# Optimization experiments

Hardware: AMD Instinct MI355X
Metric: run time of the kernel (lower is better)

Reference implementation:

```python
import jax, jax.numpy as jnp
import numpy as np

# Static config (matches init_kwargs)
B = 1
D = 1024          # model_dim
H = 16            # num_heads
HD = 64           # head_dim
TPF = 256         # tokens_per_frame = latent_height*latent_width
LH, LW = 16, 16
FRAMES = 13
PREFIX = 1
ATTN = 3
CHUNKS = 4
TXT = 226                 # text_length per chunk
SEQ_TXT = CHUNKS * TXT    # 904
VID_LEN = FRAMES * TPF    # 3328
CHUNK_VID = (PREFIX + ATTN) * TPF  # 1024 video tokens per attention chunk
THETA = 10000.0
EPS = 1e-6
SCALE = 1.0 / np.sqrt(HD)
DT, DHE, DW = 16, 24, 24  # 3D rope split of head_dim


def setup_inputs() -> dict:
    key = jax.random.key(0)
    ks = jax.random.split(key, 16)
    def w(k, shape, s=0.02):
        return (jax.random.normal(k, shape) * s).astype(jnp.float32)
    return dict(
        vid_emb=jax.random.normal(ks[0], (B, VID_LEN, D), jnp.float32),
        text_emb=jax.random.normal(ks[1], (B, SEQ_TXT, D), jnp.float32),
        Wq=w(ks[2], (D, D)), bq=jnp.zeros((D,), jnp.float32),
        Wk=w(ks[3], (D, D)), bk=jnp.zeros((D,), jnp.float32),
        Wv=w(ks[4], (D, D)), bv=jnp.zeros((D,), jnp.float32),
        Wo=w(ks[5], (D, D)), bo=jnp.zeros((D,), jnp.float32),
        qn_w=jnp.ones((HD,), jnp.float32), qn_b=jnp.zeros((HD,), jnp.float32),
        kn_w=jnp.ones((HD,), jnp.float32), kn_b=jnp.zeros((HD,), jnp.float32),
        ssm_Win=w(ks[6], (D, D)), ssm_Wout=w(ks[7], (D, D)),
        ssm_gate=jnp.zeros((D,), jnp.float32),
        fg_t=jnp.full((D,), 0.1, jnp.float32), fg_v=jnp.full((D,), 0.1, jnp.float32),
        bg_t=jnp.full((D,), 0.1, jnp.float32), bg_v=jnp.full((D,), 0.1, jnp.float32),
    )


def _layernorm(x, w, b):
    mu = jnp.mean(x, axis=-1, keepdims=True)
    var = jnp.mean((x - mu) ** 2, axis=-1, keepdims=True)
    return (x - mu) * jax.lax.rsqrt(var + EPS) * w + b


def _rope_angles():
    # per-video-token 3D positions within a chunk
    tok = jnp.arange(CHUNK_VID)
    f = (tok // TPF).astype(jnp.float32)
    rem = tok % TPF
    hp = (rem // LW).astype(jnp.float32)
    wp = (rem % LW).astype(jnp.float32)
    def inv(d):
        return THETA ** (-jnp.arange(0, d, 2, dtype=jnp.float32) / d)
    return f[:, None] * inv(DT), hp[:, None] * inv(DHE), wp[:, None] * inv(DW)


def _rot(x, ang):
    half = x.shape[-1] // 2
    c, s = jnp.cos(ang), jnp.sin(ang)
    x1, x2 = x[..., :half], x[..., half:]
    return jnp.concatenate([x1 * c - x2 * s, x1 * s + x2 * c], axis=-1)


def _apply_rope3d(x, angs):
    at, ah, aw = angs
    return jnp.concatenate([
        _rot(x[..., :DT], at),
        _rot(x[..., DT:DT + DHE], ah),
        _rot(x[..., DT + DHE:], aw),
    ], axis=-1)


def _attn_forward(vid_emb, text_emb, Wq, bq, Wk, bk, Wv, bv, Wo, bo, qn_w, qn_b, kn_w, kn_b):
    b = vid_emb.shape[0]
    starts = np.arange(CHUNKS) * ATTN * TPF
    idx = jnp.asarray(starts)[:, None] + jnp.arange(CHUNK_VID)[None, :]  # [C, CHUNK_VID]
    txt_chunks = text_emb.reshape(b, CHUNKS, TXT, D)
    vid_chunks = vid_emb[:, idx]                                          # [b, C, CHUNK_VID, D]
    cur = jnp.concatenate([txt_chunks, vid_chunks], axis=2)               # [b, C, T, D]
    T = TXT + CHUNK_VID
    cur = cur.reshape(b * CHUNKS, T, D)

    def heads(x):
        return x.reshape(b * CHUNKS, T, H, HD).transpose(0, 2, 1, 3)      # [bc, h, t, d]

    q = _layernorm(heads(cur @ Wq + bq), qn_w, qn_b)
    k = _layernorm(heads(cur @ Wk + bk), kn_w, kn_b)
    v = heads(cur @ Wv + bv)

    angs = _rope_angles()
    q = jnp.concatenate([q[:, :, :TXT], _apply_rope3d(q[:, :, TXT:], angs)], axis=2)
    k = jnp.concatenate([k[:, :, :TXT], _apply_rope3d(k[:, :, TXT:], angs)], axis=2)

    scores = jnp.einsum('bhqd,bhkd->bhqk', q, k) * SCALE
    attn = jax.nn.softmax(scores, axis=-1)
    out = jnp.einsum('bhqk,bhkd->bhqd', attn, v)
    out = out.transpose(0, 2, 1, 3).reshape(b * CHUNKS, T, D) @ Wo + bo
    out = out.reshape(b, CHUNKS, T, D)

    text_out = out[:, :, :TXT].reshape(b, SEQ_TXT, D)
    vid_part = out[:, :, TXT:]                                            # [b, C, CHUNK_VID, D]
    vid_acc = jnp.zeros((b, VID_LEN, D), vid_emb.dtype).at[:, idx].add(vid_part)
    cnt = jnp.zeros((b, VID_LEN, 1), vid_emb.dtype).at[:, idx].add(jnp.ones((b, CHUNKS, CHUNK_VID, 1), vid_emb.dtype))
    vid_out = vid_acc / cnt
    return jnp.concatenate([text_out, vid_out], axis=1)


def _ssm(x, Win, Wout, gate_logit):
    # simplified TTT stand-in: gated linear recurrence h_t = g*h_{t-1} + u_t (causal scan)
    g = jax.nn.sigmoid(gate_logit)
    u = x @ Win
    a = jnp.broadcast_to(g, u.shape)
    def comb(c1, c2):
        a1, b1 = c1
        a2, b2 = c2
        return a1 * a2, a2 * b1 + b2
    _, h = jax.lax.associative_scan(comb, (a, u), axis=1)
    return h @ Wout


def _rev_text_chunks(t):
    b = t.shape[0]
    return jnp.flip(t.reshape(b, CHUNKS, TXT, D), axis=1).reshape(b, SEQ_TXT, D)


def _ssm_forward(emb, ssm_Win, ssm_Wout, ssm_gate, fg_t, fg_v, bg_t, bg_v):
    Ttxt = SEQ_TXT
    res = emb
    y = _ssm(emb, ssm_Win, ssm_Wout, ssm_gate)
    emb = res + jnp.concatenate([jnp.tanh(fg_t) * y[:, :Ttxt], jnp.tanh(fg_v) * y[:, Ttxt:]], axis=1)
    res2 = emb
    # multiscene reverse: flip text chunk order and video token order
    rev = jnp.concatenate([_rev_text_chunks(emb[:, :Ttxt]), jnp.flip(emb[:, Ttxt:], axis=1)], axis=1)
    y2 = _ssm(rev, ssm_Win, ssm_Wout, ssm_gate)
    y2 = jnp.concatenate([_rev_text_chunks(y2[:, :Ttxt]), jnp.flip(y2[:, Ttxt:], axis=1)], axis=1)
    return res2 + jnp.concatenate([jnp.tanh(bg_t) * y2[:, :Ttxt], jnp.tanh(bg_v) * y2[:, Ttxt:]], axis=1)


def reference(vid_emb, text_emb, Wq, bq, Wk, bk, Wv, bv, Wo, bo, qn_w, qn_b, kn_w, kn_b,
              ssm_Win, ssm_Wout, ssm_gate, fg_t, fg_v, bg_t, bg_v):
    emb = _attn_forward(vid_emb, text_emb, Wq, bq, Wk, bk, Wv, bv, Wo, bo, qn_w, qn_b, kn_w, kn_b)
    out = _ssm_forward(emb, ssm_Win, ssm_Wout, ssm_gate, fg_t, fg_v, bg_t, bg_v)
    return out[:, SEQ_TXT:], out[:, :SEQ_TXT]
```

## Files before the change

kernel.cpp:

```cpp
#include <hip/hip_runtime.h>
#include <cstdint>

constexpr int Dm       = 1024;
constexpr int Hh       = 16;
constexpr int HD       = 64;
constexpr int CHUNKS   = 4;
constexpr int TXT      = 226;
constexpr int SEQ_TXT  = 904;
constexpr int VID_LEN  = 3328;
constexpr int CHUNK_VID= 1024;
constexpr int Tt       = 1250;
constexpr int Tp       = 1280;
constexpr int M_QKV    = 5000;
constexpr int SEQm     = 4232;
constexpr int STRIDE_V = 768;
constexpr float EPSc   = 1e-6f;
constexpr float SCALEc = 0.125f;
constexpr float THETAc = 10000.f;
constexpr float OFFS   = 8.0f;

constexpr int SEGL = 128;
constexpr int NSEG = (SEQm + SEGL - 1) / SEGL;

typedef __attribute__((ext_vector_type(8))) short bf16x8;
typedef __attribute__((ext_vector_type(4))) float f32x4;

__device__ __forceinline__ ushort f2bf(float x) {
    uint32_t u = __float_as_uint(x);
    u += 0x7FFFu + ((u >> 16) & 1u);
    return (ushort)(u >> 16);
}
__device__ __forceinline__ float bf2f(ushort b) {
    return __uint_as_float(((uint32_t)b) << 16);
}

__device__ __forceinline__ void gload_lds16(const ushort* g, ushort* l) {
    __builtin_amdgcn_global_load_lds(
        (const __attribute__((address_space(1))) unsigned int*)g,
        (__attribute__((address_space(3))) unsigned int*)l, 16, 0, 0);
}

__device__ __forceinline__ int rev_map(int i) {
    if (i < SEQ_TXT) {
        int c = i / TXT, o = i - c * TXT;
        return (CHUNKS - 1 - c) * TXT + o;
    }
    int j = i - SEQ_TXT;
    return SEQ_TXT + (VID_LEN - 1 - j);
}

__global__ __launch_bounds__(256) void conv_w_all(
    const float* __restrict__ Wq, const float* __restrict__ Wk,
    const float* __restrict__ Wv, const float* __restrict__ Wo,
    const float* __restrict__ Win, const float* __restrict__ Wout,
    ushort* __restrict__ WqkvH, ushort* __restrict__ WqkvL,
    ushort* __restrict__ WoH, ushort* __restrict__ WoL,
    ushort* __restrict__ WinH, ushort* __restrict__ WinL,
    ushort* __restrict__ WoutH, ushort* __restrict__ WoutL) {
    const float* W; ushort* Thi; ushort* Tlo;
    switch (blockIdx.z) {
        case 0: W = Wq;  Thi = WqkvH;               Tlo = WqkvL;               break;
        case 1: W = Wk;  Thi = WqkvH + 1024*1024;   Tlo = WqkvL + 1024*1024;   break;
        case 2: W = Wv;  Thi = WqkvH + 2*1024*1024; Tlo = WqkvL + 2*1024*1024; break;
        case 3: W = Wo;  Thi = WoH;   Tlo = WoL;   break;
        case 4: W = Win; Thi = WinH;  Tlo = WinL;  break;
        default:W = Wout;Thi = WoutH; Tlo = WoutL; break;
    }
    __shared__ float tile[32][33];
    int k0 = blockIdx.y * 32, n0 = blockIdx.x * 32;
    int j = threadIdx.x & 31, i0 = threadIdx.x >> 5;
#pragma unroll
    for (int i = i0; i < 32; i += 8)
        tile[i][j] = W[(size_t)(k0 + i) * 1024 + n0 + j];
    __syncthreads();
#pragma unroll
    for (int i = i0; i < 32; i += 8) {
        float v = tile[j][i];
        ushort h = f2bf(v);
        size_t o = (size_t)(n0 + i) * 1024 + k0 + j;
        Thi[o] = h;
        Tlo[o] = f2bf(v - bf2f(h));
    }
}

__global__ __launch_bounds__(256) void build_cur(
    const float* __restrict__ vid, const float* __restrict__ txt,
    ushort* __restrict__ chi, ushort* __restrict__ clo) {
    int idx = blockIdx.x * 256 + threadIdx.x;
    int row = idx >> 8, c4 = (idx & 255) * 4;
    int c = row / Tt, t = row - c * Tt;
    float4 x;
    if (t < TXT)
        x = *(const float4*)(txt + (size_t)(c * TXT + t) * Dm + c4);
    else
        x = *(const float4*)(vid + (size_t)(c * STRIDE_V + (t - TXT)) * Dm + c4);
    float v[4] = {x.x, x.y, x.z, x.w};
    ushort4 h, l;
    h.x = f2bf(v[0]); l.x = f2bf(v[0] - bf2f(h.x));
    h.y = f2bf(v[1]); l.y = f2bf(v[1] - bf2f(h.y));
    h.z = f2bf(v[2]); l.z = f2bf(v[2] - bf2f(h.z));
    h.w = f2bf(v[3]); l.w = f2bf(v[3] - bf2f(h.w));
    *(ushort4*)(chi + (size_t)row * Dm + c4) = h;
    *(ushort4*)(clo + (size_t)row * Dm + c4) = l;
}

template<int MODE>
__global__ __launch_bounds__(256) void gemm_sk(
    const ushort* __restrict__ Ahi, const ushort* __restrict__ Alo,
    const ushort* __restrict__ Bhi, const ushort* __restrict__ Blo,
    const float* __restrict__ f1, const float* __restrict__ f2,
    const float* __restrict__ f3,
    const ushort* __restrict__ r1, const ushort* __restrict__ r2,
    float* __restrict__ Cf, ushort* __restrict__ u1, ushort* __restrict__ u2,
    int M, int N) {
    __shared__ ushort AHL[128 * 64];
    __shared__ ushort BHL[128 * 64];
    const int tid = threadIdx.x;
    const int w = tid >> 6, lane = tid & 63;
    const int lrow = lane & 15, quad = lane >> 4;
    const int mBase = blockIdx.y * 128, nBase = blockIdx.x * 128;

    const bool isB = (w >= 2);
    const int half = w & 1;
    const ushort* Phi = isB ? Bhi : Ahi;
    const ushort* Plo = isB ? Blo : Alo;
    ushort* lds = (isB ? BHL : AHL) + half * 4096;
    const int baseR = (isB ? nBase : mBase) + half * 64;
    const int maxr = (isB ? N : M) - 1;
    const int rl8 = lane >> 3;
    const int c = (lane & 7) ^ rl8;
    const ushort* Psel = (c < 4) ? Phi : Plo;
    const ushort* gb[8];
#pragma unroll
    for (int u = 0; u < 8; ++u) {
        int rg = min(baseR + u * 8 + rl8, maxr);
        gb[u] = Psel + (size_t)rg * 1024 + (c & 3) * 8;
    }

    const int mo = (w >> 1) * 64, no = (w & 1) * 64;
    const int p = quad ^ (lrow & 7);
    f32x4 acc[4][4];
#pragma unroll
    for (int i = 0; i < 4; ++i)
#pragma unroll
        for (int j = 0; j < 4; ++j) acc[i][j] = (f32x4){0.f, 0.f, 0.f, 0.f};

    for (int kk = 0; kk < 1024; kk += 32) {
        __syncthreads();
#pragma unroll
        for (int u = 0; u < 8; ++u) gload_lds16(gb[u] + kk, lds + u * 512);
        __syncthreads();

        bf16x8 ah[4], al[4], bh[4], bl[4];
#pragma unroll
        for (int i = 0; i < 4; ++i) {
            int m = mo + i * 16 + lrow;
            ah[i] = *(const bf16x8*)&AHL[m * 64 + p * 8];
            al[i] = *(const bf16x8*)&AHL[m * 64 + (p ^ 4) * 8];
        }
#pragma unroll
        for (int j = 0; j < 4; ++j) {
            int n = no + j * 16 + lrow;
            bh[j] = *(const bf16x8*)&BHL[n * 64 + p * 8];
            bl[j] = *(const bf16x8*)&BHL[n * 64 + (p ^ 4) * 8];
        }
#pragma unroll
        for (int i = 0; i < 4; ++i)
#pragma unroll
            for (int j = 0; j < 4; ++j) {
                f32x4 a = acc[i][j];
                a = __builtin_amdgcn_mfma_f32_16x16x32_bf16(ah[i], bh[j], a, 0, 0, 0);
                a = __builtin_amdgcn_mfma_f32_16x16x32_bf16(al[i], bh[j], a, 0, 0, 0);
                a = __builtin_amdgcn_mfma_f32_16x16x32_bf16(ah[i], bl[j], a, 0, 0, 0);
                acc[i][j] = a;
            }
    }

#pragma unroll
    for (int i = 0; i < 4; ++i)
#pragma unroll
        for (int j = 0; j < 4; ++j) {
            const int col = nBase + no + j * 16 + lrow;
            float bv = 0.f, tg_t = 0.f, tg_v = 0.f;
            if constexpr (MODE == 0) bv = f1[col];
            if constexpr (MODE == 1)
                bv = (col < 1024) ? f1[col]
                   : (col < 2048) ? f2[col - 1024] : f3[col - 2048];
            if constexpr (MODE == 3 || MODE == 4) {
                tg_t = tanhf(f1[col]);
                tg_v = tanhf(f2[col]);
            }
#pragma unroll
            for (int r = 0; r < 4; ++r) {
                const int row = mBase + mo + i * 16 + quad * 4 + r;
                if (row >= M) continue;
                const size_t idx = (size_t)row * N + col;
                const float a = acc[i][j][r];
                if constexpr (MODE == 0) {
                    Cf[idx] = a + bv;
                } else if constexpr (MODE == 1) {
                    u1[idx] = f2bf(a + bv);
                } else if constexpr (MODE == 2) {
                    Cf[idx] = a;
                } else if constexpr (MODE == 3) {
                    float e = bf2f(r1[idx]) + bf2f(r2[idx]);
                    float g = (row < SEQ_TXT) ? tg_t : tg_v;
                    float v = e + g * a;
                    Cf[idx] = v;
                    ushort hh = f2bf(v);
                    u1[idx] = hh;
                    u2[idx] = f2bf(v - bf2f(hh));
                } else {
                    float e = f3[idx];
                    float g = (row < SEQ_TXT) ? tg_t : tg_v;
                    int drow = (row >= SEQ_TXT) ? (row - SEQ_TXT) : (VID_LEN + row);
                    Cf[(size_t)drow * N + col] = e + g * a;
                }
            }
        }
}

__global__ __launch_bounds__(256) void lnrope(
    const ushort* __restrict__ qkvb,
    const float* __restrict__ qn_w, const float* __restrict__ qn_b,
    const float* __restrict__ kn_w, const float* __restrict__ kn_b,
    ushort* __restrict__ qP, ushort* __restrict__ kP, ushort* __restrict__ vT) {
    __shared__ ushort vtile[64][72];
    const int ch = blockIdx.y, c = ch >> 4, h = ch & 15;
    const int t0 = blockIdx.x * 64;
    const int tid = threadIdx.x, w = tid >> 6, lane = tid & 63;

    auto wsum = [](float x) {
#pragma unroll
        for (int o = 32; o; o >>= 1) x += __shfl_xor(x, o);
        return x;
    };

#pragma unroll 1
    for (int it = 0; it < 16; ++it) {
        const int tl = w * 16 + it;
        const int t = t0 + tl;
        ushort qb = 0, kb = 0, vb = 0;
        if (t < Tt) {
            size_t src = (size_t)(c * Tt + t) * 3072 + h * HD + lane;
            float qv = bf2f(qkvb[src]);
            float kv = bf2f(qkvb[src + 1024]);
            float vv = bf2f(qkvb[src + 2048]);

            float qmu = wsum(qv) * (1.f / 64.f);
            float qd  = qv - qmu;
            float qvar = wsum(qd * qd) * (1.f / 64.f);
            float qn = qd * rsqrtf(qvar + EPSc) * qn_w[lane] + qn_b[lane];

            float kmu = wsum(kv) * (1.f / 64.f);
            float kd  = kv - kmu;
            float kvar = wsum(kd * kd) * (1.f / 64.f);
            float kn = kd * rsqrtf(kvar + EPSc) * kn_w[lane] + kn_b[lane];

            if (t >= TXT) {
                int pos = t - TXT;
                int f = pos >> 8, rem2 = pos & 255, hp = rem2 >> 4, wp = rem2 & 15;
                int dim, pp, dl;
                if (lane < 16)      { dim = 16; pp = f;  dl = lane; }
                else if (lane < 40) { dim = 24; pp = hp; dl = lane - 16; }
                else                { dim = 24; pp = wp; dl = lane - 40; }
                int halfd = dim >> 1;
                int i = (dl < halfd) ? dl : dl - halfd;
                float ang = (float)pp * powf(THETAc, -2.0f * (float)i / (float)dim);
                float cs = cosf(ang), sn = sinf(ang);
                int partner = (dl < halfd) ? (lane + halfd) : (lane - halfd);
                float qo = __shfl(qn, partner);
                float ko = __shfl(kn, partner);
                qn = (dl < halfd) ? (qn * cs - qo * sn) : (qo * sn + qn * cs);
                kn = (dl < halfd) ? (kn * cs - ko * sn) : (ko * sn + kn * cs);
            }
            qb = f2bf(qn * SCALEc);
            kb = f2bf(kn);
            vb = f2bf(vv);
        }
        size_t dst = ((size_t)ch * Tp + t) * HD + lane;
        qP[dst] = qb;
        kP[dst] = kb;
        vtile[tl][lane] = vb;
    }
    __syncthreads();
    const int r = tid >> 2, ck = tid & 3;
    ushort* dst = vT + ((size_t)ch * HD + r) * Tp + t0;
    short o1[8], o2[8];
#pragma unroll
    for (int j = 0; j < 8; ++j) {
        o1[j] = (short)vtile[ck * 8 + j][r];
        o2[j] = (short)vtile[(ck + 4) * 8 + j][r];
    }
    *(bf16x8*)(dst + ck * 8)       = *(bf16x8*)o1;
    *(bf16x8*)(dst + (ck + 4) * 8) = *(bf16x8*)o2;
}

__global__ __launch_bounds__(256) void attn_mfma(
    const ushort* __restrict__ qP, const ushort* __restrict__ kP,
    const ushort* __restrict__ vT,
    ushort* __restrict__ ohi, ushort* __restrict__ olo) {
    const int ch = blockIdx.y;
    const int c = ch >> 4, h = ch & 15;
    const int qbase = blockIdx.x * 64;
    const int tid = threadIdx.x, w = tid >> 6, lane = tid & 63;
    const int lrow = lane & 15, quad = lane >> 4;

    __shared__ ushort KT[2][32 * 64];
    __shared__ ushort VTs[2][64 * 32];
    __shared__ ushort PB[4][16][40];

    const ushort* kg = kP + (size_t)ch * Tp * HD;
    const ushort* vg = vT + (size_t)ch * HD * Tp;

    const ushort* kgl = kg + (size_t)(w * 8 + (lane >> 3)) * HD
                           + ((lane & 7) ^ ((lane >> 3) & 7)) * 8;
    const ushort* vgl = vg + (size_t)(w * 16 + (lane >> 2)) * Tp + (lane & 3) * 8;

    const int qr = qbase + w * 16 + lrow;
    const ushort* qgp = qP + ((size_t)ch * Tp + qr) * HD + quad * 8;
    bf16x8 qf0 = *(const bf16x8*)qgp;
    bf16x8 qf1 = *(const bf16x8*)(qgp + 32);

    f32x4 accO[4];
#pragma unroll
    for (int dt = 0; dt < 4; ++dt) accO[dt] = (f32x4){0.f, 0.f, 0.f, 0.f};
    float lacc[4] = {0.f, 0.f, 0.f, 0.f};

    gload_lds16(kgl, &KT[0][w * 512]);
    gload_lds16(vgl, &VTs[0][w * 512]);

    const int NSTEP = Tp / 32;
    for (int s = 0; s < NSTEP; ++s) {
        const int b = s & 1;
        __syncthreads();
        if (s + 1 < NSTEP) {
            int kb = (s + 1) * 32;
            gload_lds16(kgl + (size_t)kb * HD, &KT[1 - b][w * 512]);
            gload_lds16(vgl + kb, &VTs[1 - b][w * 512]);
        }

        const int sw = lrow & 7;
        const ushort* r0 = &KT[b][lrow * 64];
        const ushort* r1 = &KT[b][(16 + lrow) * 64];
        bf16x8 k00 = *(const bf16x8*)(r0 + (quad ^ sw) * 8);
        bf16x8 k01 = *(const bf16x8*)(r0 + ((4 + quad) ^ sw) * 8);
        bf16x8 k10 = *(const bf16x8*)(r1 + (quad ^ sw) * 8);
        bf16x8 k11 = *(const bf16x8*)(r1 + ((4 + quad) ^ sw) * 8);
        f32x4 s0 = (f32x4){0.f, 0.f, 0.f, 0.f}, s1 = s0;
        s0 = __builtin_amdgcn_mfma_f32_16x16x32_bf16(qf0, k00, s0, 0, 0, 0);
        s0 = __builtin_amdgcn_mfma_f32_16x16x32_bf16(qf1, k01, s0, 0, 0, 0);
        s1 = __builtin_amdgcn_mfma_f32_16x16x32_bf16(qf0, k10, s1, 0, 0, 0);
        s1 = __builtin_amdgcn_mfma_f32_16x16x32_bf16(qf1, k11, s1, 0, 0, 0);

#pragma unroll
        for (int r = 0; r < 4; ++r) {
            float p0 = __expf(s0[r] - OFFS);
            float p1 = __expf(s1[r] - OFFS);
            lacc[r] += p0 + p1;
            int row = quad * 4 + r;
            PB[w][row][lrow]      = f2bf(p0);
            PB[w][row][16 + lrow] = f2bf(p1);
        }

        bf16x8 pf = *(const bf16x8*)&PB[w][lrow][quad * 8];
#pragma unroll
        for (int dt = 0; dt < 4; ++dt) {
            bf16x8 vf = *(const bf16x8*)&VTs[b][(dt * 16 + lrow) * 32 + quad * 8];
            accO[dt] = __builtin_amdgcn_mfma_f32_16x16x32_bf16(pf, vf, accO[dt], 0, 0, 0);
        }
    }

    float il[4];
#pragma unroll
    for (int r = 0; r < 4; ++r) {
        float l = lacc[r];
        l += __shfl_xor(l, 1);
        l += __shfl_xor(l, 2);
        l += __shfl_xor(l, 4);
        l += __shfl_xor(l, 8);
        l -= (float)(Tp - Tt) * __expf(-OFFS);
        il[r] = 1.f / l;
    }
#pragma unroll
    for (int dt = 0; dt < 4; ++dt)
#pragma unroll
        for (int r = 0; r < 4; ++r) {
            int qrow = qbase + w * 16 + quad * 4 + r;
            if (qrow < Tt) {
                float val = accO[dt][r] * il[r];
                size_t o = (size_t)(c * Tt + qrow) * Dm + h * HD + dt * 16 + lrow;
                ushort hv = f2bf(val);
                ohi[o] = hv;
                olo[o] = f2bf(val - bf2f(hv));
            }
        }
}

__global__ __launch_bounds__(256) void scatter_emb(
    const float* __restrict__ proj,
    ushort* __restrict__ ehi, ushort* __restrict__ elo) {
    int idx = blockIdx.x * 256 + threadIdx.x;
    int row = idx >> 8, c4 = (idx & 255) * 4;
    float4 o;
    if (row < SEQ_TXT) {
        int c = row / TXT, t = row - c * TXT;
        o = *(const float4*)(proj + (size_t)(c * Tt + t) * Dm + c4);
    } else {
        int p = row - SEQ_TXT;
        float sx = 0.f, sy = 0.f, sz = 0.f, sw = 0.f; int cnt = 0;
#pragma unroll
        for (int c = 0; c < CHUNKS; ++c) {
            int off = p - c * STRIDE_V;
            if (off >= 0 && off < CHUNK_VID) {
                float4 x = *(const float4*)(proj + (size_t)(c * Tt + TXT + off) * Dm + c4);
                sx += x.x; sy += x.y; sz += x.z; sw += x.w; ++cnt;
            }
        }
        float inv = 1.f / (float)cnt;
        o = make_float4(sx * inv, sy * inv, sz * inv, sw * inv);
    }
    float v[4] = {o.x, o.y, o.z, o.w};
    ushort4 h, l;
    h.x = f2bf(v[0]); l.x = f2bf(v[0] - bf2f(h.x));
    h.y = f2bf(v[1]); l.y = f2bf(v[1] - bf2f(h.y));
    h.z = f2bf(v[2]); l.z = f2bf(v[2] - bf2f(h.z));
    h.w = f2bf(v[3]); l.w = f2bf(v[3] - bf2f(h.w));
    *(ushort4*)(ehi + (size_t)row * Dm + c4) = h;
    *(ushort4*)(elo + (size_t)row * Dm + c4) = l;
}

__global__ __launch_bounds__(256) void scan_carry(
    const float* __restrict__ u, const float* __restrict__ gate,
    float* __restrict__ carry, int perm) {
    int ch = blockIdx.x * 256 + threadIdx.x;
    int seg = blockIdx.y;
    float g = 1.f / (1.f + expf(-gate[ch]));
    int t0 = seg * SEGL, t1 = min(SEQm, t0 + SEGL);
    float hv = 0.f;
    for (int t = t0; t < t1; ++t) {
        int rt = perm ? rev_map(t) : t;
        hv = fmaf(g, hv, u[(size_t)rt * Dm + ch]);
    }
    carry[(size_t)seg * Dm + ch] = hv;
}

__global__ __launch_bounds__(256) void scan_combine(
    const float* __restrict__ carry, const float* __restrict__ gate,
    float* __restrict__ inc) {
    int ch = blockIdx.x * 256 + threadIdx.x;
    float g = 1.f / (1.f + expf(-gate[ch]));
    float gl = powf(g, (float)SEGL);
    float S = 0.f;
    for (int s = 0; s < NSEG; ++s) {
        inc[(size_t)s * Dm + ch] = S;
        int len = min(SEGL, SEQm - s * SEGL);
        float A = (len == SEGL) ? gl : powf(g, (float)len);
        S = fmaf(A, S, carry[(size_t)s * Dm + ch]);
    }
}

__global__ __launch_bounds__(256) void scan_final(
    const float* __restrict__ u, const float* __restrict__ gate,
    const float* __restrict__ inc,
    ushort* __restrict__ hhi, ushort* __restrict__ hlo, int perm) {
    int ch = blockIdx.x * 256 + threadIdx.x;
    int seg = blockIdx.y;
    float g = 1.f / (1.f + expf(-gate[ch]));
    int t0 = seg * SEGL, t1 = min(SEQm, t0 + SEGL);
    float hv = inc[(size_t)seg * Dm + ch];
    for (int t = t0; t < t1; ++t) {
        int rt = perm ? rev_map(t) : t;
        hv = fmaf(g, hv, u[(size_t)rt * Dm + ch]);
        ushort h = f2bf(hv);
        hhi[(size_t)rt * Dm + ch] = h;
        hlo[(size_t)rt * Dm + ch] = f2bf(hv - bf2f(h));
    }
}

extern "C" void kernel_launch(void* const* d_in, const int* in_sizes, int n_in,
                              void* d_out, int out_size, void* d_ws, size_t ws_size,
                              hipStream_t stream) {
    const float* vid_emb = (const float*)d_in[0];
    const float* text_emb= (const float*)d_in[1];
    const float* Wq = (const float*)d_in[2];  const float* bq = (const float*)d_in[3];
    const float* Wk = (const float*)d_in[4];  const float* bk = (const float*)d_in[5];
    const float* Wv = (const float*)d_in[6];  const float* bv = (const float*)d_in[7];
    const float* Wo = (const float*)d_in[8];  const float* bo = (const float*)d_in[9];
    const float* qn_w = (const float*)d_in[10]; const float* qn_b = (const float*)d_in[11];
    const float* kn_w = (const float*)d_in[12]; const float* kn_b = (const float*)d_in[13];
    const float* Win  = (const float*)d_in[14]; const float* Wout = (const float*)d_in[15];
    const float* gate = (const float*)d_in[16];
    const float* fg_t = (const float*)d_in[17]; const float* fg_v = (const float*)d_in[18];
    const float* bg_t = (const float*)d_in[19]; const float* bg_v = (const float*)d_in[20];

    char* W8 = (char*)d_ws;
    if (ws_size < 132284416u) return;
    ushort* WqkvH = (ushort*)(W8 + 0);
    ushort* WqkvL = (ushort*)(W8 + 6291456);
    ushort* WoH   = (ushort*)(W8 + 12582912);
    ushort* WoL   = (ushort*)(W8 + 14680064);
    ushort* WinH  = (ushort*)(W8 + 16777216);
    ushort* WinL  = (ushort*)(W8 + 18874368);
    ushort* WoutH = (ushort*)(W8 + 20971520);
    ushort* WoutL = (ushort*)(W8 + 23068672);
    ushort* qkvb  = (ushort*)(W8 + 25165824);
    ushort* curH  = (ushort*)(W8 + 55885824);
    ushort* curL  = (ushort*)(W8 + 66125824);
    ushort* qPl   = (ushort*)(W8 + 76365824);
    ushort* kPl   = (ushort*)(W8 + 86851584);
    ushort* vTl   = (ushort*)(W8 + 97337344);
    ushort* aoutH = (ushort*)(W8 + 25165824);
    ushort* aoutL = (ushort*)(W8 + 35405824);
    float*  proj  = (float*) (W8 + 55885824);
    ushort* embH  = (ushort*)(W8 + 25165824);
    ushort* embL  = (ushort*)(W8 + 33832960);
    float*  u     = (float*) (W8 + 55885824);
    ushort* hbufH = (ushort*)(W8 + 76365824);
    ushort* hbufL = (ushort*)(W8 + 85032960);
    float*  emb2  = (float*) (W8 + 97337344);
    ushort* e2H   = (ushort*)(W8 + 114671616);
    ushort* e2L   = (ushort*)(W8 + 123338752);
    float*  carry = (float*) (W8 + 132005888);
    float*  incb  = (float*) (W8 + 132145152);
    float*  outp  = (float*)d_out;

    conv_w_all<<<dim3(32, 32, 6), 256, 0, stream>>>(
        Wq, Wk, Wv, Wo, Win, Wout,
        WqkvH, WqkvL, WoH, WoL, WinH, WinL, WoutH, WoutL);

    build_cur<<<M_QKV, 256, 0, stream>>>(vid_emb, text_emb, curH, curL);

    gemm_sk<1><<<dim3(24, 40), 256, 0, stream>>>(
        curH, curL, WqkvH, WqkvL, bq, bk, bv, nullptr, nullptr,
        nullptr, qkvb, nullptr, M_QKV, 3072);

    lnrope<<<dim3(Tp / 64, 64), 256, 0, stream>>>(qkvb, qn_w, qn_b, kn_w, kn_b,
                                                  qPl, kPl, vTl);

    attn_mfma<<<dim3(Tp / 64, 64), 256, 0, stream>>>(qPl, kPl, vTl, aoutH, aoutL);

    gemm_sk<0><<<dim3(8, 40), 256, 0, stream>>>(
        aoutH, aoutL, WoH, WoL, bo, nullptr, nullptr, nullptr, nullptr,
        proj, nullptr, nullptr, M_QKV, 1024);

    scatter_emb<<<SEQm, 256, 0, stream>>>(proj, embH, embL);

    dim3 gsq(8, 34);
    dim3 gscan(Dm / 256, NSEG);

    gemm_sk<2><<<gsq, 256, 0, stream>>>(
        embH, embL, WinH, WinL, nullptr, nullptr, nullptr, nullptr, nullptr,
        u, nullptr, nullptr, SEQm, 1024);
    scan_carry<<<gscan, 256, 0, stream>>>(u, gate, carry, 0);
    scan_combine<<<Dm / 256, 256, 0, stream>>>(carry, gate, incb);
    scan_final<<<gscan, 256, 0, stream>>>(u, gate, incb, hbufH, hbufL, 0);
    gemm_sk<3><<<gsq, 256, 0, stream>>>(
        hbufH, hbufL, WoutH, WoutL, fg_t, fg_v, nullptr, embH, embL,
        emb2, e2H, e2L, SEQm, 1024);

    gemm_sk<2><<<gsq, 256, 0, stream>>>(
        e2H, e2L, WinH, WinL, nullptr, nullptr, nullptr, nullptr, nullptr,
        u, nullptr, nullptr, SEQm, 1024);
    scan_carry<<<gscan, 256, 0, stream>>>(u, gate, carry, 1);
    scan_combine<<<Dm / 256, 256, 0, stream>>>(carry, gate, incb);
    scan_final<<<gscan, 256, 0, stream>>>(u, gate, incb, hbufH, hbufL, 1);
    gemm_sk<4><<<gsq, 256, 0, stream>>>(
        hbufH, hbufL, WoutH, WoutL, bg_t, bg_v, emb2, nullptr, nullptr,
        outp, nullptr, nullptr, SEQm, 1024);
}
```

Before: 774.6 us.

## Split-K the N=1024 GEMMs in two and fold reductions into epilogue kernels

The 1024-wide GEMMs (Wo, SSM Win and Wout) now run as split-K with two K halves on blockIdx.z, each writing its own fp32 partial buffer. This doubles the grid from about 272-320 to 544-640 blocks so the many CUs stay busy. The partial sums are added inside the consumers: scan_carry and scan_final, a new reduce_scatter that also adds the bias, and new reduce_c1 and reduce_fin kernels that apply the gated residual. The cost is an extra fp32 partial write and read, and two more launches. The workspace buffers are remapped to fit the larger partials.

```diff
diff --git a/kernel.cpp b/kernel.cpp
--- a/kernel.cpp
+++ b/kernel.cpp
@@ -110,8 +110,7 @@
     const ushort* __restrict__ Bhi, const ushort* __restrict__ Blo,
     const float* __restrict__ f1, const float* __restrict__ f2,
     const float* __restrict__ f3,
-    const ushort* __restrict__ r1, const ushort* __restrict__ r2,
-    float* __restrict__ Cf, ushort* __restrict__ u1, ushort* __restrict__ u2,
+    float* __restrict__ Cf, ushort* __restrict__ u1,
     int M, int N) {
     __shared__ ushort AHL[128 * 64];
     __shared__ ushort BHL[128 * 64];
@@ -145,7 +144,9 @@
 #pragma unroll
         for (int j = 0; j < 4; ++j) acc[i][j] = (f32x4){0.f, 0.f, 0.f, 0.f};
 
-    for (int kk = 0; kk < 1024; kk += 32) {
+    const int kk0 = (MODE == 5) ? blockIdx.z * 512 : 0;
+    const int kk1 = (MODE == 5) ? kk0 + 512 : 1024;
+    for (int kk = kk0; kk < kk1; kk += 32) {
         __syncthreads();
 #pragma unroll
         for (int u = 0; u < 8; ++u) gload_lds16(gb[u] + kk, lds + u * 512);
@@ -176,45 +177,26 @@
             }
     }
 
+    const size_t zoff = (MODE == 5) ? (size_t)blockIdx.z * M * N : 0;
 #pragma unroll
     for (int i = 0; i < 4; ++i)
 #pragma unroll
         for (int j = 0; j < 4; ++j) {
             const int col = nBase + no + j * 16 + lrow;
-            float bv = 0.f, tg_t = 0.f, tg_v = 0.f;
-            if constexpr (MODE == 0) bv = f1[col];
+            float bv = 0.f;
             if constexpr (MODE == 1)
                 bv = (col < 1024) ? f1[col]
                    : (col < 2048) ? f2[col - 1024] : f3[col - 2048];
-            if constexpr (MODE == 3 || MODE == 4) {
-                tg_t = tanhf(f1[col]);
-                tg_v = tanhf(f2[col]);
-            }
 #pragma unroll
             for (int r = 0; r < 4; ++r) {
                 const int row = mBase + mo + i * 16 + quad * 4 + r;
                 if (row >= M) continue;
                 const size_t idx = (size_t)row * N + col;
                 const float a = acc[i][j][r];
-                if constexpr (MODE == 0) {
-                    Cf[idx] = a + bv;
-                } else if constexpr (MODE == 1) {
+                if constexpr (MODE == 1) {
                     u1[idx] = f2bf(a + bv);
-                } else if constexpr (MODE == 2) {
-                    Cf[idx] = a;
-                } else if constexpr (MODE == 3) {
-                    float e = bf2f(r1[idx]) + bf2f(r2[idx]);
-                    float g = (row < SEQ_TXT) ? tg_t : tg_v;
-                    float v = e + g * a;
-                    Cf[idx] = v;
-                    ushort hh = f2bf(v);
-                    u1[idx] = hh;
-                    u2[idx] = f2bf(v - bf2f(hh));
                 } else {
-                    float e = f3[idx];
-                    float g = (row < SEQ_TXT) ? tg_t : tg_v;
-                    int drow = (row >= SEQ_TXT) ? (row - SEQ_TXT) : (VID_LEN + row);
-                    Cf[(size_t)drow * N + col] = e + g * a;
+                    Cf[zoff + idx] = a;
                 }
             }
         }
@@ -397,30 +379,39 @@
         }
 }
 
-__global__ __launch_bounds__(256) void scatter_emb(
-    const float* __restrict__ proj,
+__global__ __launch_bounds__(256) void reduce_scatter(
+    const float* __restrict__ P0, const float* __restrict__ bo,
     ushort* __restrict__ ehi, ushort* __restrict__ elo) {
+    const float* P1 = P0 + (size_t)M_QKV * Dm;
     int idx = blockIdx.x * 256 + threadIdx.x;
     int row = idx >> 8, c4 = (idx & 255) * 4;
-    float4 o;
+    float sx, sy, sz, sw;
     if (row < SEQ_TXT) {
         int c = row / TXT, t = row - c * TXT;
-        o = *(const float4*)(proj + (size_t)(c * Tt + t) * Dm + c4);
+        size_t o = (size_t)(c * Tt + t) * Dm + c4;
+        float4 a = *(const float4*)(P0 + o);
+        float4 b = *(const float4*)(P1 + o);
+        sx = a.x + b.x; sy = a.y + b.y; sz = a.z + b.z; sw = a.w + b.w;
     } else {
         int p = row - SEQ_TXT;
-        float sx = 0.f, sy = 0.f, sz = 0.f, sw = 0.f; int cnt = 0;
+        sx = sy = sz = sw = 0.f; int cnt = 0;
 #pragma unroll
         for (int c = 0; c < CHUNKS; ++c) {
             int off = p - c * STRIDE_V;
             if (off >= 0 && off < CHUNK_VID) {
-                float4 x = *(const float4*)(proj + (size_t)(c * Tt + TXT + off) * Dm + c4);
-                sx += x.x; sy += x.y; sz += x.z; sw += x.w; ++cnt;
+                size_t o = (size_t)(c * Tt + TXT + off) * Dm + c4;
+                float4 a = *(const float4*)(P0 + o);
+                float4 b = *(const float4*)(P1 + o);
+                sx += a.x + b.x; sy += a.y + b.y;
+                sz += a.z + b.z; sw += a.w + b.w;
+                ++cnt;
             }
         }
         float inv = 1.f / (float)cnt;
-        o = make_float4(sx * inv, sy * inv, sz * inv, sw * inv);
-    }
-    float v[4] = {o.x, o.y, o.z, o.w};
+        sx *= inv; sy *= inv; sz *= inv; sw *= inv;
+    }
+    float4 b4 = *(const float4*)(bo + c4);
+    float v[4] = {sx + b4.x, sy + b4.y, sz + b4.z, sw + b4.w};
     ushort4 h, l;
     h.x = f2bf(v[0]); l.x = f2bf(v[0] - bf2f(h.x));
     h.y = f2bf(v[1]); l.y = f2bf(v[1] - bf2f(h.y));
@@ -431,8 +422,9 @@
 }
 
 __global__ __launch_bounds__(256) void scan_carry(
-    const float* __restrict__ u, const float* __restrict__ gate,
+    const float* __restrict__ P0, const float* __restrict__ gate,
     float* __restrict__ carry, int perm) {
+    const float* P1 = P0 + (size_t)SEQm * Dm;
     int ch = blockIdx.x * 256 + threadIdx.x;
     int seg = blockIdx.y;
     float g = 1.f / (1.f + expf(-gate[ch]));
@@ -440,7 +432,8 @@
     float hv = 0.f;
     for (int t = t0; t < t1; ++t) {
         int rt = perm ? rev_map(t) : t;
-        hv = fmaf(g, hv, u[(size_t)rt * Dm + ch]);
+        size_t o = (size_t)rt * Dm + ch;
+        hv = fmaf(g, hv, P0[o] + P1[o]);
     }
     carry[(size_t)seg * Dm + ch] = hv;
 }
@@ -461,9 +454,10 @@
 }
 
 __global__ __launch_bounds__(256) void scan_final(
-    const float* __restrict__ u, const float* __restrict__ gate,
+    const float* __restrict__ P0, const float* __restrict__ gate,
     const float* __restrict__ inc,
     ushort* __restrict__ hhi, ushort* __restrict__ hlo, int perm) {
+    const float* P1 = P0 + (size_t)SEQm * Dm;
     int ch = blockIdx.x * 256 + threadIdx.x;
     int seg = blockIdx.y;
     float g = 1.f / (1.f + expf(-gate[ch]));
@@ -471,11 +465,61 @@
     float hv = inc[(size_t)seg * Dm + ch];
     for (int t = t0; t < t1; ++t) {
         int rt = perm ? rev_map(t) : t;
-        hv = fmaf(g, hv, u[(size_t)rt * Dm + ch]);
+        size_t o = (size_t)rt * Dm + ch;
+        hv = fmaf(g, hv, P0[o] + P1[o]);
         ushort h = f2bf(hv);
-        hhi[(size_t)rt * Dm + ch] = h;
-        hlo[(size_t)rt * Dm + ch] = f2bf(hv - bf2f(h));
-    }
+        hhi[o] = h;
+        hlo[o] = f2bf(hv - bf2f(h));
+    }
+}
+
+__global__ __launch_bounds__(256) void reduce_c1(
+    const float* __restrict__ P0,
+    const ushort* __restrict__ ehi, const ushort* __restrict__ elo,
+    const float* __restrict__ fg_t, const float* __restrict__ fg_v,
+    float* __restrict__ emb2, ushort* __restrict__ e2hi, ushort* __restrict__ e2lo) {
+    const float* P1 = P0 + (size_t)SEQm * Dm;
+    int idx = blockIdx.x * 256 + threadIdx.x;
+    int row = idx >> 8, c4 = (idx & 255) * 4;
+    const float* fg = (row < SEQ_TXT) ? fg_t : fg_v;
+    size_t o = (size_t)row * Dm + c4;
+    float4 a = *(const float4*)(P0 + o);
+    float4 b = *(const float4*)(P1 + o);
+    ushort4 eh = *(const ushort4*)(ehi + o);
+    ushort4 el = *(const ushort4*)(elo + o);
+    float v[4];
+    v[0] = (bf2f(eh.x) + bf2f(el.x)) + tanhf(fg[c4 + 0]) * (a.x + b.x);
+    v[1] = (bf2f(eh.y) + bf2f(el.y)) + tanhf(fg[c4 + 1]) * (a.y + b.y);
+    v[2] = (bf2f(eh.z) + bf2f(el.z)) + tanhf(fg[c4 + 2]) * (a.z + b.z);
+    v[3] = (bf2f(eh.w) + bf2f(el.w)) + tanhf(fg[c4 + 3]) * (a.w + b.w);
+    *(float4*)(emb2 + o) = make_float4(v[0], v[1], v[2], v[3]);
+    ushort4 h, l;
+    h.x = f2bf(v[0]); l.x = f2bf(v[0] - bf2f(h.x));
+    h.y = f2bf(v[1]); l.y = f2bf(v[1] - bf2f(h.y));
+    h.z = f2bf(v[2]); l.z = f2bf(v[2] - bf2f(h.z));
+    h.w = f2bf(v[3]); l.w = f2bf(v[3] - bf2f(h.w));
+    *(ushort4*)(e2hi + o) = h;
+    *(ushort4*)(e2lo + o) = l;
+}
+
+__global__ __launch_bounds__(256) void reduce_fin(
+    const float* __restrict__ P0, const float* __restrict__ emb2,
+    const float* __restrict__ bg_t, const float* __restrict__ bg_v,
+    float* __restrict__ outp) {
+    const float* P1 = P0 + (size_t)SEQm * Dm;
+    int idx = blockIdx.x * 256 + threadIdx.x;
+    int row = idx >> 8, c4 = (idx & 255) * 4;
+    const float* bg = (row < SEQ_TXT) ? bg_t : bg_v;
+    int drow = (row >= SEQ_TXT) ? (row - SEQ_TXT) : (VID_LEN + row);
+    size_t o = (size_t)row * Dm + c4;
+    float4 a = *(const float4*)(P0 + o);
+    float4 b = *(const float4*)(P1 + o);
+    float4 e = *(const float4*)(emb2 + o);
+    float4 r = make_float4(e.x + tanhf(bg[c4 + 0]) * (a.x + b.x),
+                           e.y + tanhf(bg[c4 + 1]) * (a.y + b.y),
+                           e.z + tanhf(bg[c4 + 2]) * (a.z + b.z),
+                           e.w + tanhf(bg[c4 + 3]) * (a.w + b.w));
+    *(float4*)(outp + (size_t)drow * Dm + c4) = r;
 }
 
 extern "C" void kernel_launch(void* const* d_in, const int* in_sizes, int n_in,
@@ -512,17 +556,19 @@
     ushort* vTl   = (ushort*)(W8 + 97337344);
     ushort* aoutH = (ushort*)(W8 + 25165824);
     ushort* aoutL = (ushort*)(W8 + 35405824);
-    float*  proj  = (float*) (W8 + 55885824);
-    ushort* embH  = (ushort*)(W8 + 25165824);
-    ushort* embL  = (ushort*)(W8 + 33832960);
-    float*  u     = (float*) (W8 + 55885824);
-    ushort* hbufH = (ushort*)(W8 + 76365824);
-    ushort* hbufL = (ushort*)(W8 + 85032960);
-    float*  emb2  = (float*) (W8 + 97337344);
-    ushort* e2H   = (ushort*)(W8 + 114671616);
-    ushort* e2L   = (ushort*)(W8 + 123338752);
-    float*  carry = (float*) (W8 + 132005888);
-    float*  incb  = (float*) (W8 + 132145152);
+    float*  PWo   = (float*) (W8 + 76365824);
+    ushort* embH  = (ushort*)(W8 + 45645824);
+    ushort* embL  = (ushort*)(W8 + 54312960);
+    float*  PW    = (float*) (W8 + 76365824);
+    ushort* hbufH = (ushort*)(W8 + 25165824);
+    ushort* hbufL = (ushort*)(W8 + 33832960);
+    float*  emb2  = (float*) (W8 + 111034368);
+    ushort* e2H   = (ushort*)(W8 + 25165824);
+    ushort* e2L   = (ushort*)(W8 + 33832960);
+    ushort* hbuf2H= (ushort*)(W8 + 45645824);
+    ushort* hbuf2L= (ushort*)(W8 + 54312960);
+    float*  carry = (float*) (W8 + 128368640);
+    float*  incb  = (float*) (W8 + 128507904);
     float*  outp  = (float*)d_out;
 
     conv_w_all<<<dim3(32, 32, 6), 256, 0, stream>>>(
@@ -532,40 +578,41 @@
     build_cur<<<M_QKV, 256, 0, stream>>>(vid_emb, text_emb, curH, curL);
 
     gemm_sk<1><<<dim3(24, 40), 256, 0, stream>>>(
-        curH, curL, WqkvH, WqkvL, bq, bk, bv, nullptr, nullptr,
-        nullptr, qkvb, nullptr, M_QKV, 3072);
+        curH, curL, WqkvH, WqkvL, bq, bk, bv, nullptr, qkvb, M_QKV, 3072);
 
     lnrope<<<dim3(Tp / 64, 64), 256, 0, stream>>>(qkvb, qn_w, qn_b, kn_w, kn_b,
                                                   qPl, kPl, vTl);
 
     attn_mfma<<<dim3(Tp / 64, 64), 256, 0, stream>>>(qPl, kPl, vTl, aoutH, aoutL);
 
-    gemm_sk<0><<<dim3(8, 40), 256, 0, stream>>>(
-        aoutH, aoutL, WoH, WoL, bo, nullptr, nullptr, nullptr, nullptr,
-        proj, nullptr, nullptr, M_QKV, 1024);
-
-    scatter_emb<<<SEQm, 256, 0, stream>>>(proj, embH, embL);
-
-    dim3 gsq(8, 34);
+    gemm_sk<5><<<dim3(8, 40, 2), 256, 0, stream>>>(
+        aoutH, aoutL, WoH, WoL, nullptr, nullptr, nullptr, PWo, nullptr,
+        M_QKV, 1024);
+    reduce_scatter<<<SEQm, 256, 0, stream>>>(PWo, bo, embH, embL);
+
+    dim3 gsq(8, 34, 2);
     dim3 gscan(Dm / 256, NSEG);
 
-    gemm_sk<2><<<gsq, 256, 0, stream>>>(
-        embH, embL, WinH, WinL, nullptr, nullptr, nullptr, nullptr, nullptr,
-        u, nullptr, nullptr, SEQm, 1024);
-    scan_carry<<<gscan, 256, 0, stream>>>(u, gate, carry, 0);
+    gemm_sk<5><<<gsq, 256, 0, stream>>>(
+        embH, embL, WinH, WinL, nullptr, nullptr, nullptr, PW, nullptr,
+        SEQm, 1024);
+    scan_carry<<<gscan, 256, 0, stream>>>(PW, gate, carry, 0);
     scan_combine<<<Dm / 256, 256, 0, stream>>>(carry, gate, incb);
-    scan_final<<<gscan, 256, 0, stream>>>(u, gate, incb, hbufH, hbufL, 0);
-    gemm_sk<3><<<gsq, 256, 0, stream>>>(
-        hbufH, hbufL, WoutH, WoutL, fg_t, fg_v, nullptr, embH, embL,
-        emb2, e2H, e2L, SEQm, 1024);
-
-    gemm_sk<2><<<gsq, 256, 0, stream>>>(
-        e2H, e2L, WinH, WinL, nullptr, nullptr, nullptr, nullptr, nullptr,
-        u, nullptr, nullptr, SEQm, 1024);
-    scan_carry<<<gscan, 256, 0, stream>>>(u, gate, carry, 1);
+    scan_final<<<gscan, 256, 0, stream>>>(PW, gate, incb, hbufH, hbufL, 0);
+    gemm_sk<5><<<gsq, 256, 0, stream>>>(
+        hbufH, hbufL, WoutH, WoutL, nullptr, nullptr, nullptr, PW, nullptr,
+        SEQm, 1024);
+    reduce_c1<<<SEQm, 256, 0, stream>>>(PW, embH, embL, fg_t, fg_v,
+                                        emb2, e2H, e2L);
+
+    gemm_sk<5><<<gsq, 256, 0, stream>>>(
+        e2H, e2L, WinH, WinL, nullptr, nullptr, nullptr, PW, nullptr,
+        SEQm, 1024);
+    scan_carry<<<gscan, 256, 0, stream>>>(PW, gate, carry, 1);
     scan_combine<<<Dm / 256, 256, 0, stream>>>(carry, gate, incb);
-    scan_final<<<gscan, 256, 0, stream>>>(u, gate, incb, hbufH, hbufL, 1);
-    gemm_sk<4><<<gsq, 256, 0, stream>>>(
-        hbufH, hbufL, WoutH, WoutL, bg_t, bg_v, emb2, nullptr, nullptr,
-        outp, nullptr, nullptr, SEQm, 1024);
-}
+    scan_final<<<gscan, 256, 0, stream>>>(PW, gate, incb, hbuf2H, hbuf2L, 1);
+    gemm_sk<5><<<gsq, 256, 0, stream>>>(
+        hbuf2H, hbuf2L, WoutH, WoutL, nullptr, nullptr, nullptr, PW, nullptr,
+        SEQm, 1024);
+    reduce_fin<<<SEQm, 256, 0, stream>>>(PW, emb2, bg_t, bg_v, outp);
+}
```

Result: no change. 779.7 us (+0.7%).
